# Kernel tuning notes

Measured on AMD Instinct MI355X. Metric: run time of the kernel, lower is better.

The kernel has to match this reference:

```python
import jax, jax.numpy as jnp
import numpy as np

K = 4  # number of processing steps (init kwarg)


def setup_inputs() -> dict:
    key = jax.random.key(0)
    ks = jax.random.split(key, 6)
    B, S, D = 4096, 8192, 512
    H = D  # hidden_size == input_size (residual h + f_x)
    scale = 1.0 / np.sqrt(H)
    return {
        "f_x": jax.random.normal(ks[0], (B, D), dtype=jnp.float32),
        "g_S": jax.random.normal(ks[1], (S, D), dtype=jnp.float32),
        # LSTM step: input f_x (size D), 'hidden' is concat([h, r]) of size 2H
        "W_ih": jax.random.uniform(ks[2], (4 * H, D), jnp.float32, -scale, scale),
        "W_hh": jax.random.uniform(ks[3], (4 * H, 2 * H), jnp.float32, -scale, scale),
        "b_ih": jax.random.uniform(ks[4], (4 * H,), jnp.float32, -scale, scale),
        "b_hh": jax.random.uniform(ks[5], (4 * H,), jnp.float32, -scale, scale),
    }


def _lstm_step(x, hidden, c, W_ih, W_hh, b_ih, b_hh):
    # gates: [B, 4H]; PyTorch LSTMCell gate order (i, f, g, o)
    gates = x @ W_ih.T + b_ih + hidden @ W_hh.T + b_hh
    i, f, g, o = jnp.split(gates, 4, axis=1)
    c_new = jax.nn.sigmoid(f) * c + jax.nn.sigmoid(i) * jnp.tanh(g)
    h_new = jax.nn.sigmoid(o) * jnp.tanh(c_new)
    return h_new, c_new


def reference(f_x, g_S, W_ih, W_hh, b_ih, b_hh):
    # f_x: [B, D] queries; g_S: [S, D] support set embeddings
    h = f_x
    c = jnp.zeros_like(f_x)
    for _ in range(K):
        a = jax.nn.softmax(h @ g_S.T, axis=1)       # [B, S] attention over support
        r = a @ g_S                                  # [B, D] attention readout
        concat = jnp.concatenate([h, r], axis=1)     # [B, 2D]
        h, c = _lstm_step(f_x, concat, c, W_ih, W_hh, b_ih, b_hh)
        h = h + f_x                                  # residual skip connection
    return h
```

## Files before the change

### kernel.cpp

```cpp
#include <hip/hip_runtime.h>

typedef _Float16 f16x8 __attribute__((ext_vector_type(8)));
typedef _Float16 f16x4 __attribute__((ext_vector_type(4)));
typedef float f32x4 __attribute__((ext_vector_type(4)));

#define S_DIM 8192
#define D_DIM 512

__device__ __forceinline__ void gload_lds16(const _Float16* g, _Float16* l) {
  __builtin_amdgcn_global_load_lds(
      (const __attribute__((address_space(1))) unsigned int*)g,
      (__attribute__((address_space(3))) unsigned int*)l, 16, 0, 0);
}

__device__ __forceinline__ float sigf(float x) { return 1.0f / (1.0f + __expf(-x)); }
__device__ __forceinline__ float tanhfast(float x) {
  return 1.0f - 2.0f / (__expf(2.0f * x) + 1.0f);
}


template <int BM, int BN>
__global__ __launch_bounds__(256) void gemm_bt(const _Float16* __restrict__ A, int lda,
                                               const _Float16* __restrict__ B, int ldb,
                                               _Float16* __restrict__ C, int ldc, int K) {
  constexpr int BK = 64;
  constexpr int FM = BM / 32, FN = BN / 32;
  __shared__ _Float16 As[BM * BK];
  __shared__ _Float16 Bs[BN * BK];
  const int tid = threadIdx.x;
  const int lane = tid & 63;
  const int wv = tid >> 6;
  const int bm = blockIdx.y * BM;
  const int bn = blockIdx.x * BN;
  const int wm = (wv >> 1) * (BM / 2);
  const int wn = (wv & 1) * (BN / 2);
  const int fr = lane & 15;
  const int hi4 = lane >> 4;
  const int rx7 = fr & 7;
  const int srow = lane >> 3;
  const int schk = (lane & 7) ^ srow;

  f32x4 acc[FM][FN] = {};

  for (int kt = 0; kt < K; kt += BK) {
    __syncthreads();
#pragma unroll
    for (int p = 0; p < BM / 32; ++p) {
      const int m = wv + 4 * p;
      gload_lds16(A + (size_t)(bm + 8 * m + srow) * lda + kt + schk * 8, As + 512 * m);
    }
#pragma unroll
    for (int p = 0; p < BN / 32; ++p) {
      const int m = wv + 4 * p;
      gload_lds16(B + (size_t)(bn + 8 * m + srow) * ldb + kt + schk * 8, Bs + 512 * m);
    }
    __syncthreads();

#pragma unroll
    for (int h = 0; h < 2; ++h) {
      const int co = (((h << 2) | hi4) ^ rx7) << 3;
      f16x8 af[FM], bf[FN];
#pragma unroll
      for (int i = 0; i < FM; ++i)
        af[i] = *(const f16x8*)&As[(wm + i * 16 + fr) * 64 + co];
#pragma unroll
      for (int j = 0; j < FN; ++j)
        bf[j] = *(const f16x8*)&Bs[(wn + j * 16 + fr) * 64 + co];
#pragma unroll
      for (int i = 0; i < FM; ++i)
#pragma unroll
        for (int j = 0; j < FN; ++j)
          acc[i][j] = __builtin_amdgcn_mfma_f32_16x16x32_f16(af[i], bf[j], acc[i][j], 0, 0, 0);
    }
  }

  const int cc = lane & 15;
  const int cr = (lane >> 4) * 4;
#pragma unroll
  for (int i = 0; i < FM; ++i)
#pragma unroll
    for (int j = 0; j < FN; ++j) {
      size_t base = (size_t)(bm + wm + i * 16 + cr) * ldc + (bn + wn + j * 16 + cc);
#pragma unroll
      for (int r = 0; r < 4; ++r) C[base + (size_t)r * ldc] = (_Float16)acc[i][j][r];
    }
}

__global__ __launch_bounds__(256) void gemm_rsplit(const _Float16* __restrict__ A,
                                                   const _Float16* __restrict__ B,
                                                   float* __restrict__ Ppart) {
  constexpr int BK = 64;
  __shared__ _Float16 As[128 * BK];
  __shared__ _Float16 Bs[64 * BK];
  const int tid = threadIdx.x;
  const int lane = tid & 63;
  const int wv = tid >> 6;
  const int bm = blockIdx.x * 128;
  const int bn = blockIdx.y * 64;
  const int kc = blockIdx.z;
  const int k0 = kc * 1024;
  const int wm = (wv >> 1) * 64;
  const int wn = (wv & 1) * 32;
  const int fr = lane & 15;
  const int hi4 = lane >> 4;
  const int rx7 = fr & 7;
  const int srow = lane >> 3;
  const int schk = (lane & 7) ^ srow;

  f32x4 acc[4][2] = {};

  for (int kt = k0; kt < k0 + 1024; kt += BK) {
    __syncthreads();
#pragma unroll
    for (int p = 0; p < 4; ++p) {
      const int m = wv + 4 * p;
      gload_lds16(A + (size_t)(bm + 8 * m + srow) * 16384 + kt + schk * 8, As + 512 * m);
    }
#pragma unroll
    for (int p = 0; p < 2; ++p) {
      const int m = wv + 4 * p;
      gload_lds16(B + (size_t)(bn + 8 * m + srow) * 8192 + kt + schk * 8, Bs + 512 * m);
    }
    __syncthreads();

#pragma unroll
    for (int h = 0; h < 2; ++h) {
      const int co = (((h << 2) | hi4) ^ rx7) << 3;
      f16x8 af[4], bf[2];
#pragma unroll
      for (int i = 0; i < 4; ++i)
        af[i] = *(const f16x8*)&As[(wm + i * 16 + fr) * 64 + co];
#pragma unroll
      for (int j = 0; j < 2; ++j)
        bf[j] = *(const f16x8*)&Bs[(wn + j * 16 + fr) * 64 + co];
#pragma unroll
      for (int i = 0; i < 4; ++i)
#pragma unroll
        for (int j = 0; j < 2; ++j)
          acc[i][j] = __builtin_amdgcn_mfma_f32_16x16x32_f16(af[i], bf[j], acc[i][j], 0, 0, 0);
    }
  }

  const int cc = lane & 15;
  const int cr = (lane >> 4) * 4;
#pragma unroll
  for (int i = 0; i < 4; ++i)
#pragma unroll
    for (int j = 0; j < 2; ++j) {
      size_t base = (size_t)(bm + wm + i * 16 + cr) * 8192 + 4096 + (size_t)kc * 512 +
                    (bn + wn + j * 16 + cc);
#pragma unroll
      for (int r = 0; r < 4; ++r) Ppart[base + (size_t)r * 8192] = acc[i][j][r];
    }
}

__global__ __launch_bounds__(256) void reduce_r(const float* __restrict__ Ppart,
                                                _Float16* __restrict__ rout) {
  int idx = blockIdx.x * 256 + threadIdx.x;
  int m = idx >> 7;
  int n4 = (idx & 127) * 4;
  const float* base = Ppart + (size_t)m * 8192 + 4096 + n4;
  f32x4 s = {0.f, 0.f, 0.f, 0.f};
#pragma unroll
  for (int kc = 0; kc < 8; ++kc) s += *(const f32x4*)(base + kc * 512);
  f16x4 h = {(_Float16)s[0], (_Float16)s[1], (_Float16)s[2], (_Float16)s[3]};
  *(f16x4*)&rout[(size_t)m * 1024 + n4] = h;
}

__global__ __launch_bounds__(256) void gemm_scores(const _Float16* __restrict__ Ah, int ldah,
                                                   const _Float16* __restrict__ Al,
                                                   const _Float16* __restrict__ Bh,
                                                   float* __restrict__ C) {
  constexpr int BK = 64;
  __shared__ _Float16 AsH[128 * BK];
  __shared__ _Float16 AsL[128 * BK];
  __shared__ _Float16 BsH[128 * BK];
  const int tid = threadIdx.x;
  const int lane = tid & 63;
  const int wv = tid >> 6;
  const int bm = blockIdx.y * 128;
  const int bn = blockIdx.x * 128;
  const int wm = (wv >> 1) * 64;
  const int wn = (wv & 1) * 64;
  const int fr = lane & 15;
  const int hi4 = lane >> 4;
  const int rx7 = fr & 7;
  const int srow = lane >> 3;
  const int schk = (lane & 7) ^ srow;

  f32x4 acc[4][4] = {};

  for (int kt = 0; kt < 512; kt += BK) {
    __syncthreads();
#pragma unroll
    for (int p = 0; p < 4; ++p) {
      const int m = wv + 4 * p;
      const int row = 8 * m + srow;
      gload_lds16(Ah + (size_t)(bm + row) * ldah + kt + schk * 8, AsH + 512 * m);
      gload_lds16(Al + (size_t)(bm + row) * 512 + kt + schk * 8, AsL + 512 * m);
      gload_lds16(Bh + (size_t)(bn + row) * 512 + kt + schk * 8, BsH + 512 * m);
    }
    __syncthreads();

#pragma unroll
    for (int h = 0; h < 2; ++h) {
      const int co = (((h << 2) | hi4) ^ rx7) << 3;
      f16x8 fah[4], fal[4], fbh[4];
#pragma unroll
      for (int i = 0; i < 4; ++i) {
        fah[i] = *(const f16x8*)&AsH[(wm + i * 16 + fr) * 64 + co];
        fal[i] = *(const f16x8*)&AsL[(wm + i * 16 + fr) * 64 + co];
        fbh[i] = *(const f16x8*)&BsH[(wn + i * 16 + fr) * 64 + co];
      }
#pragma unroll
      for (int i = 0; i < 4; ++i)
#pragma unroll
        for (int j = 0; j < 4; ++j) {
          acc[i][j] = __builtin_amdgcn_mfma_f32_16x16x32_f16(fah[i], fbh[j], acc[i][j], 0, 0, 0);
          acc[i][j] = __builtin_amdgcn_mfma_f32_16x16x32_f16(fal[i], fbh[j], acc[i][j], 0, 0, 0);
        }
    }
  }

  const int cc = lane & 15;
  const int cr = (lane >> 4) * 4;
#pragma unroll
  for (int i = 0; i < 4; ++i)
#pragma unroll
    for (int j = 0; j < 4; ++j) {
      size_t base = (size_t)(bm + wm + i * 16 + cr) * 8192 + (bn + wn + j * 16 + cc);
#pragma unroll
      for (int r = 0; r < 4; ++r) C[base + (size_t)r * 8192] = acc[i][j][r];
    }
}

__global__ __launch_bounds__(256) void prep_g(const float* __restrict__ g,
                                              _Float16* __restrict__ gT,
                                              _Float16* __restrict__ g_h) {
  __shared__ _Float16 tile[64][72];
  const int s0 = blockIdx.x * 64;
  const int d0 = blockIdx.y * 64;
  const int t = threadIdx.x;
  const int r = t >> 2;
  const int cq = (t & 3) * 16;
  alignas(16) _Float16 buf[16];
#pragma unroll
  for (int q = 0; q < 4; ++q) {
    f32x4 v = *(const f32x4*)&g[(size_t)(s0 + r) * D_DIM + d0 + cq + q * 4];
#pragma unroll
    for (int e = 0; e < 4; ++e) buf[q * 4 + e] = (_Float16)v[e];
  }
#pragma unroll
  for (int k = 0; k < 16; ++k) tile[r][cq + k] = buf[k];
  *(f16x8*)&g_h[(size_t)(s0 + r) * D_DIM + d0 + cq] = *(const f16x8*)&buf[0];
  *(f16x8*)&g_h[(size_t)(s0 + r) * D_DIM + d0 + cq + 8] = *(const f16x8*)&buf[8];
  __syncthreads();
  alignas(16) _Float16 ob[16];
#pragma unroll
  for (int k = 0; k < 16; ++k) ob[k] = tile[cq + k][r];
  *(f16x8*)&gT[(size_t)(d0 + r) * S_DIM + s0 + cq] = *(const f16x8*)&ob[0];
  *(f16x8*)&gT[(size_t)(d0 + r) * S_DIM + s0 + cq + 8] = *(const f16x8*)&ob[8];
}

__global__ __launch_bounds__(256) void prep_misc(const float* __restrict__ W_ih,
                                                 const float* __restrict__ W_hh,
                                                 const float* __restrict__ f_x,
                                                 _Float16* __restrict__ wih_h,
                                                 _Float16* __restrict__ whh_h,
                                                 _Float16* __restrict__ concat,
                                                 _Float16* __restrict__ h_lo,
                                                 float* __restrict__ c) {
  const int NW1 = 2048 * 512 / 4;
  const int NW2 = 2048 * 1024 / 4;
  const int NFX = 4096 * 512 / 4;
  int idx = blockIdx.x * 256 + threadIdx.x;
  if (idx < NW1) {
    f32x4 v = ((const f32x4*)W_ih)[idx];
    f16x4 h = {(_Float16)v[0], (_Float16)v[1], (_Float16)v[2], (_Float16)v[3]};
    ((f16x4*)wih_h)[idx] = h;
  } else if (idx < NW1 + NW2) {
    int k = idx - NW1;
    f32x4 v = ((const f32x4*)W_hh)[k];
    f16x4 h = {(_Float16)v[0], (_Float16)v[1], (_Float16)v[2], (_Float16)v[3]};
    ((f16x4*)whh_h)[k] = h;
  } else if (idx < NW1 + NW2 + NFX) {
    int k = idx - NW1 - NW2;
    f32x4 v = ((const f32x4*)f_x)[k];
    f16x4 h, lo;
#pragma unroll
    for (int e = 0; e < 4; ++e) {
      h[e] = (_Float16)v[e];
      lo[e] = (_Float16)(v[e] - (float)h[e]);
    }
    int m = k >> 7, j4 = k & 127;
    ((f16x4*)concat)[m * 256 + j4] = h;
    ((f16x4*)h_lo)[k] = lo;
    f32x4 z = {0.f, 0.f, 0.f, 0.f};
    ((f32x4*)c)[k] = z;
  }
}

__global__ __launch_bounds__(256) void softmax_inplace(float* __restrict__ P) {
  float* p = P + (size_t)blockIdx.x * S_DIM;
  const int tid = threadIdx.x, lane = tid & 63, wave = tid >> 6;
  __shared__ float red[8];
  float x[32];
#pragma unroll
  for (int i = 0; i < 8; ++i) {
    f32x4 v = *(const f32x4*)&p[i * 1024 + tid * 4];
#pragma unroll
    for (int j = 0; j < 4; ++j) x[i * 4 + j] = v[j];
  }
  float m = -3.0e38f;
#pragma unroll
  for (int k = 0; k < 32; ++k) m = fmaxf(m, x[k]);
#pragma unroll
  for (int o = 32; o; o >>= 1) m = fmaxf(m, __shfl_xor(m, o));
  if (lane == 0) red[wave] = m;
  __syncthreads();
  m = fmaxf(fmaxf(red[0], red[1]), fmaxf(red[2], red[3]));
  float s = 0.f;
#pragma unroll
  for (int k = 0; k < 32; ++k) {
    x[k] = exp2f((x[k] - m) * 1.44269504f);
    s += x[k];
  }
#pragma unroll
  for (int o = 32; o; o >>= 1) s += __shfl_xor(s, o);
  if (lane == 0) red[4 + wave] = s;
  __syncthreads();
  s = (red[4] + red[5]) + (red[6] + red[7]);
  float inv = 1.0f / s;
  _Float16* out = (_Float16*)p;
#pragma unroll
  for (int i = 0; i < 8; ++i) {
    f16x4 v;
#pragma unroll
    for (int j = 0; j < 4; ++j) v[j] = (_Float16)(x[i * 4 + j] * inv);
    *(f16x4*)&out[i * 1024 + tid * 4] = v;
  }
}

__global__ __launch_bounds__(256) void lstm_step(const _Float16* __restrict__ gmm,
                                                 const _Float16* __restrict__ gbase,
                                                 const float* __restrict__ b_ih,
                                                 const float* __restrict__ b_hh,
                                                 const float* __restrict__ f_x,
                                                 float* __restrict__ c,
                                                 _Float16* __restrict__ concat,
                                                 _Float16* __restrict__ h_lo,
                                                 float* __restrict__ hout) {
  int idx = blockIdx.x * 256 + threadIdx.x;
  int m = idx >> 7;
  int j = (idx & 127) * 4;
  size_t grow = (size_t)m * 2048 + j;
  f16x4 gI = *(const f16x4*)&gmm[grow];
  f16x4 gF = *(const f16x4*)&gmm[grow + 512];
  f16x4 gG = *(const f16x4*)&gmm[grow + 1024];
  f16x4 gO = *(const f16x4*)&gmm[grow + 1536];
  f16x4 aI = *(const f16x4*)&gbase[grow];
  f16x4 aF = *(const f16x4*)&gbase[grow + 512];
  f16x4 aG = *(const f16x4*)&gbase[grow + 1024];
  f16x4 aO = *(const f16x4*)&gbase[grow + 1536];
  f32x4 biI = *(const f32x4*)&b_ih[j];
  f32x4 biF = *(const f32x4*)&b_ih[j + 512];
  f32x4 biG = *(const f32x4*)&b_ih[j + 1024];
  f32x4 biO = *(const f32x4*)&b_ih[j + 1536];
  f32x4 bhI = *(const f32x4*)&b_hh[j];
  f32x4 bhF = *(const f32x4*)&b_hh[j + 512];
  f32x4 bhG = *(const f32x4*)&b_hh[j + 1024];
  f32x4 bhO = *(const f32x4*)&b_hh[j + 1536];
  f32x4 cv = ((const f32x4*)c)[idx];
  f32x4 fx = ((const f32x4*)f_x)[idx];
  f32x4 cn, hn;
  f16x4 h16, l16;
#pragma unroll
  for (int k = 0; k < 4; ++k) {
    float gi = (float)gI[k] + (float)aI[k] + biI[k] + bhI[k];
    float gf = (float)gF[k] + (float)aF[k] + biF[k] + bhF[k];
    float gg = (float)gG[k] + (float)aG[k] + biG[k] + bhG[k];
    float go = (float)gO[k] + (float)aO[k] + biO[k] + bhO[k];
    float ci = sigf(gf) * cv[k] + sigf(gi) * tanhfast(gg);
    float hi = sigf(go) * tanhfast(ci) + fx[k];
    cn[k] = ci;
    hn[k] = hi;
    h16[k] = (_Float16)hi;
    l16[k] = (_Float16)(hi - (float)h16[k]);
  }
  ((f32x4*)c)[idx] = cn;
  ((f32x4*)hout)[idx] = hn;
  ((f16x4*)concat)[m * 256 + (idx & 127)] = h16;
  ((f16x4*)h_lo)[idx] = l16;
}

extern "C" void kernel_launch(void* const* d_in, const int* in_sizes, int n_in,
                              void* d_out, int out_size, void* d_ws, size_t ws_size,
                              hipStream_t stream) {
  const float* f_x = (const float*)d_in[0];
  const float* g_S = (const float*)d_in[1];
  const float* W_ih = (const float*)d_in[2];
  const float* W_hh = (const float*)d_in[3];
  const float* b_ih = (const float*)d_in[4];
  const float* b_hh = (const float*)d_in[5];
  float* hout = (float*)d_out;

  char* w = (char*)d_ws;
  float* P32 = (float*)w;
  _Float16* gates = (_Float16*)w;
  _Float16* gbase = (_Float16*)(w + 67108864);
  _Float16* concat = (_Float16*)(w + 83886080);
  _Float16* g_h = (_Float16*)(w + 92274688);
  _Float16* gT = (_Float16*)(w + 109051904);
  _Float16* wih_h = (_Float16*)(w + 117440512);
  _Float16* whh_h = (_Float16*)(w + 119537664);
  float* c = (float*)(w + 123731968);
  _Float16* h_lo = (_Float16*)(w + 132120576);

  prep_g<<<dim3(S_DIM / 64, D_DIM / 64), 256, 0, stream>>>(g_S, gT, g_h);
  prep_misc<<<5120, 256, 0, stream>>>(W_ih, W_hh, f_x, wih_h, whh_h, concat, h_lo, c);

  gemm_bt<128, 128><<<dim3(2048 / 128, 4096 / 128), 256, 0, stream>>>(
      concat, 1024, wih_h, 512, gbase, 2048, 512);

  for (int it = 0; it < 4; ++it) {
    for (int hb = 0; hb < 2; ++hb) {
      const _Float16* hhi = concat + (size_t)hb * 2048 * 1024;
      const _Float16* hlo = h_lo + (size_t)hb * 2048 * 512;
      gemm_scores<<<dim3(64, 16), 256, 0, stream>>>(hhi, 1024, hlo, g_h, P32);
      softmax_inplace<<<2048, 256, 0, stream>>>(P32);
      gemm_rsplit<<<dim3(16, 8, 8), 256, 0, stream>>>((const _Float16*)P32, gT, P32);
      reduce_r<<<1024, 256, 0, stream>>>(P32, concat + (size_t)hb * 2048 * 1024 + 512);
    }
    gemm_bt<128, 128><<<dim3(2048 / 128, 4096 / 128), 256, 0, stream>>>(
        concat, 1024, whh_h, 1024, gates, 2048, 1024);
    lstm_step<<<2048, 256, 0, stream>>>(gates, gbase, b_ih, b_hh, f_x, c, concat, h_lo, hout);
  }
  (void)in_sizes; (void)n_in; (void)out_size; (void)ws_size;
}
```

Baseline: 870.8 us.

## Rewrite scores GEMM with 256x256 tiles, double-buffered LDS, and split-K hi/lo stages

Replaces the scores GEMM with a 512-thread kernel using 256x256 block tiles and double-buffered LDS, so global loads for the next K-tile overlap the MFMA work on the current one. Instead of loading hi and lo A fragments together in each step, K is treated as 16 tiles: the first 8 read the hi part and the last 8 read the lo part, both against the same B. MFMA sections are wrapped in s_setprio. This reuses each B tile over more rows and hides load latency. In exchange it uses more LDS and registers and launches only 256 blocks per call, which may lower occupancy.

```diff
diff --git a/kernel.cpp b/kernel.cpp
--- a/kernel.cpp
+++ b/kernel.cpp
@@ -167,65 +167,84 @@
   *(f16x4*)&rout[(size_t)m * 1024 + n4] = h;
 }
 
-__global__ __launch_bounds__(256) void gemm_scores(const _Float16* __restrict__ Ah, int ldah,
-                                                   const _Float16* __restrict__ Al,
-                                                   const _Float16* __restrict__ Bh,
-                                                   float* __restrict__ C) {
-  constexpr int BK = 64;
-  __shared__ _Float16 AsH[128 * BK];
-  __shared__ _Float16 AsL[128 * BK];
-  __shared__ _Float16 BsH[128 * BK];
+__global__ __launch_bounds__(512) void gemm_scores2(const _Float16* __restrict__ Ah,
+                                                    const _Float16* __restrict__ Al,
+                                                    const _Float16* __restrict__ Bh,
+                                                    float* __restrict__ C) {
+  __shared__ _Float16 As[2][256 * 64];
+  __shared__ _Float16 Bs[2][256 * 64];
   const int tid = threadIdx.x;
   const int lane = tid & 63;
   const int wv = tid >> 6;
-  const int bm = blockIdx.y * 128;
-  const int bn = blockIdx.x * 128;
-  const int wm = (wv >> 1) * 64;
-  const int wn = (wv & 1) * 64;
+  const int bm = blockIdx.y * 256;
+  const int bn = blockIdx.x * 256;
+  const int wm = (wv >> 2) * 128;
+  const int wn = (wv & 3) * 64;
   const int fr = lane & 15;
   const int hi4 = lane >> 4;
   const int rx7 = fr & 7;
   const int srow = lane >> 3;
   const int schk = (lane & 7) ^ srow;
 
-  f32x4 acc[4][4] = {};
-
-  for (int kt = 0; kt < 512; kt += BK) {
+  f32x4 acc[8][4] = {};
+
+  auto stage_q = [&](int t, int q, _Float16* nA, _Float16* nB) {
+    const int m = wv + 8 * q;
+    const int k0 = t * 64;
+    const _Float16* asrc =
+        (t < 8) ? Ah + (size_t)(bm + 8 * m + srow) * 1024 + k0 + schk * 8
+                : Al + (size_t)(bm + 8 * m + srow) * 512 + (k0 - 512) + schk * 8;
+    gload_lds16(asrc, nA + 512 * m);
+    gload_lds16(Bh + (size_t)(bn + 8 * m + srow) * 512 + (t & 7) * 64 + schk * 8,
+                nB + 512 * m);
+  };
+
+  auto tile = [&](int t, const _Float16* cA, const _Float16* cB, _Float16* nA,
+                  _Float16* nB) {
+#pragma unroll
+    for (int q = 0; q < 4; ++q) {
+      if (t < 15) stage_q(t + 1, q, nA, nB);
+      f16x8 af[2][2], bf[4][2];
+#pragma unroll
+      for (int ii = 0; ii < 2; ++ii)
+#pragma unroll
+        for (int h = 0; h < 2; ++h)
+          af[ii][h] = *(const f16x8*)&cA[(wm + (2 * q + ii) * 16 + fr) * 64 +
+                                         ((((h << 2) | hi4) ^ rx7) << 3)];
+#pragma unroll
+      for (int j = 0; j < 4; ++j)
+#pragma unroll
+        for (int h = 0; h < 2; ++h)
+          bf[j][h] = *(const f16x8*)&cB[(wn + j * 16 + fr) * 64 +
+                                        ((((h << 2) | hi4) ^ rx7) << 3)];
+      __builtin_amdgcn_s_setprio(1);
+#pragma unroll
+      for (int ii = 0; ii < 2; ++ii)
+#pragma unroll
+        for (int j = 0; j < 4; ++j) {
+          acc[2 * q + ii][j] = __builtin_amdgcn_mfma_f32_16x16x32_f16(
+              af[ii][0], bf[j][0], acc[2 * q + ii][j], 0, 0, 0);
+          acc[2 * q + ii][j] = __builtin_amdgcn_mfma_f32_16x16x32_f16(
+              af[ii][1], bf[j][1], acc[2 * q + ii][j], 0, 0, 0);
+        }
+      __builtin_amdgcn_s_setprio(0);
+    }
     __syncthreads();
-#pragma unroll
-    for (int p = 0; p < 4; ++p) {
-      const int m = wv + 4 * p;
-      const int row = 8 * m + srow;
-      gload_lds16(Ah + (size_t)(bm + row) * ldah + kt + schk * 8, AsH + 512 * m);
-      gload_lds16(Al + (size_t)(bm + row) * 512 + kt + schk * 8, AsL + 512 * m);
-      gload_lds16(Bh + (size_t)(bn + row) * 512 + kt + schk * 8, BsH + 512 * m);
-    }
-    __syncthreads();
-
-#pragma unroll
-    for (int h = 0; h < 2; ++h) {
-      const int co = (((h << 2) | hi4) ^ rx7) << 3;
-      f16x8 fah[4], fal[4], fbh[4];
-#pragma unroll
-      for (int i = 0; i < 4; ++i) {
-        fah[i] = *(const f16x8*)&AsH[(wm + i * 16 + fr) * 64 + co];
-        fal[i] = *(const f16x8*)&AsL[(wm + i * 16 + fr) * 64 + co];
-        fbh[i] = *(const f16x8*)&BsH[(wn + i * 16 + fr) * 64 + co];
-      }
-#pragma unroll
-      for (int i = 0; i < 4; ++i)
-#pragma unroll
-        for (int j = 0; j < 4; ++j) {
-          acc[i][j] = __builtin_amdgcn_mfma_f32_16x16x32_f16(fah[i], fbh[j], acc[i][j], 0, 0, 0);
-          acc[i][j] = __builtin_amdgcn_mfma_f32_16x16x32_f16(fal[i], fbh[j], acc[i][j], 0, 0, 0);
-        }
-    }
+  };
+
+#pragma unroll
+  for (int q = 0; q < 4; ++q) stage_q(0, q, As[0], Bs[0]);
+  __syncthreads();
+
+  for (int tt = 0; tt < 16; tt += 2) {
+    tile(tt, As[0], Bs[0], As[1], Bs[1]);
+    tile(tt + 1, As[1], Bs[1], As[0], Bs[0]);
   }
 
   const int cc = lane & 15;
   const int cr = (lane >> 4) * 4;
 #pragma unroll
-  for (int i = 0; i < 4; ++i)
+  for (int i = 0; i < 8; ++i)
 #pragma unroll
     for (int j = 0; j < 4; ++j) {
       size_t base = (size_t)(bm + wm + i * 16 + cr) * 8192 + (bn + wn + j * 16 + cc);
@@ -426,7 +445,7 @@
     for (int hb = 0; hb < 2; ++hb) {
       const _Float16* hhi = concat + (size_t)hb * 2048 * 1024;
       const _Float16* hlo = h_lo + (size_t)hb * 2048 * 512;
-      gemm_scores<<<dim3(64, 16), 256, 0, stream>>>(hhi, 1024, hlo, g_h, P32);
+      gemm_scores2<<<dim3(32, 8), 512, 0, stream>>>(hhi, hlo, g_h, P32);
       softmax_inplace<<<2048, 256, 0, stream>>>(P32);
       gemm_rsplit<<<dim3(16, 8, 8), 256, 0, stream>>>((const _Float16*)P32, gT, P32);
       reduce_r<<<1024, 256, 0, stream>>>(P32, concat + (size_t)hb * 2048 * 1024 + 512);
```

After: 887.0 us. Within noise of the previous version (+1.9%).

## Fuse hidden-to-gates GEMM with LSTM cell update and split h/r buffers

Applied to the files above, without the earlier changes.

Replaces the separate gates GEMM and elementwise lstm_step kernel with one gemm_gates kernel. Each block computes all four gate slices for 32 hidden columns, then applies the LSTM update directly in the epilogue, so the fp16 gates tensor is never written to or read back from memory. The concat buffer is split into ping-pong h buffers plus a separate r buffer, and the two biases are pre-summed once. The fused GEMM uses 128x128 tiles with no double-buffering and scalar epilogue stores, which may cost some GEMM efficiency.

```diff
diff --git a/kernel.cpp b/kernel.cpp
--- a/kernel.cpp
+++ b/kernel.cpp
@@ -164,7 +164,7 @@
 #pragma unroll
   for (int kc = 0; kc < 8; ++kc) s += *(const f32x4*)(base + kc * 512);
   f16x4 h = {(_Float16)s[0], (_Float16)s[1], (_Float16)s[2], (_Float16)s[3]};
-  *(f16x4*)&rout[(size_t)m * 1024 + n4] = h;
+  *(f16x4*)&rout[(size_t)m * 512 + n4] = h;
 }
 
 __global__ __launch_bounds__(256) void gemm_scores(const _Float16* __restrict__ Ah, int ldah,
@@ -234,6 +234,97 @@
     }
 }
 
+__global__ __launch_bounds__(256) void gemm_gates(const _Float16* __restrict__ Ah,
+                                                  const _Float16* __restrict__ Ar,
+                                                  const _Float16* __restrict__ B,
+                                                  const _Float16* __restrict__ gbase,
+                                                  const float* __restrict__ bsum,
+                                                  const float* __restrict__ f_x,
+                                                  float* __restrict__ c,
+                                                  _Float16* __restrict__ hnext,
+                                                  _Float16* __restrict__ h_lo,
+                                                  float* __restrict__ hout) {
+  __shared__ _Float16 As[128 * 64];
+  __shared__ _Float16 Bs[128 * 64];
+  const int tid = threadIdx.x;
+  const int lane = tid & 63;
+  const int wv = tid >> 6;
+  const int n0 = blockIdx.x * 32;
+  const int bm = blockIdx.y * 128;
+  const int fr = lane & 15;
+  const int hi4 = lane >> 4;
+  const int rx7 = fr & 7;
+  const int srow = lane >> 3;
+  const int schk = (lane & 7) ^ srow;
+
+  f32x4 acc[2][8] = {};
+
+  for (int t = 0; t < 16; ++t) {
+    const int kt = t * 64;
+    __syncthreads();
+#pragma unroll
+    for (int p = 0; p < 4; ++p) {
+      const int m = wv + 4 * p;
+      const int arow = bm + 8 * m + srow;
+      const _Float16* asrc = (t < 8)
+                                 ? Ah + (size_t)arow * 512 + kt + schk * 8
+                                 : Ar + (size_t)arow * 512 + (kt - 512) + schk * 8;
+      gload_lds16(asrc, As + 512 * m);
+      const int brow = 8 * m + srow;
+      const int wrow = ((brow >> 5) << 9) + n0 + (brow & 31);
+      gload_lds16(B + (size_t)wrow * 1024 + kt + schk * 8, Bs + 512 * m);
+    }
+    __syncthreads();
+
+#pragma unroll
+    for (int h = 0; h < 2; ++h) {
+      const int co = (((h << 2) | hi4) ^ rx7) << 3;
+      f16x8 af[2], bf[8];
+#pragma unroll
+      for (int i = 0; i < 2; ++i)
+        af[i] = *(const f16x8*)&As[(wv * 32 + i * 16 + fr) * 64 + co];
+#pragma unroll
+      for (int j = 0; j < 8; ++j)
+        bf[j] = *(const f16x8*)&Bs[(j * 16 + fr) * 64 + co];
+#pragma unroll
+      for (int i = 0; i < 2; ++i)
+#pragma unroll
+        for (int j = 0; j < 8; ++j)
+          acc[i][j] = __builtin_amdgcn_mfma_f32_16x16x32_f16(af[i], bf[j], acc[i][j], 0, 0, 0);
+    }
+  }
+
+  const int cc = lane & 15;
+  const int cr = (lane >> 4) * 4;
+#pragma unroll
+  for (int jj = 0; jj < 2; ++jj) {
+    const int colq = n0 + jj * 16 + cc;
+    const float bI = bsum[colq];
+    const float bF = bsum[colq + 512];
+    const float bG = bsum[colq + 1024];
+    const float bO = bsum[colq + 1536];
+#pragma unroll
+    for (int i = 0; i < 2; ++i)
+#pragma unroll
+      for (int r = 0; r < 4; ++r) {
+        const int row = bm + wv * 32 + i * 16 + cr + r;
+        const size_t g0 = (size_t)row * 2048 + colq;
+        const float gi = acc[i][jj][r] + (float)gbase[g0] + bI;
+        const float gf = acc[i][2 + jj][r] + (float)gbase[g0 + 512] + bF;
+        const float gg = acc[i][4 + jj][r] + (float)gbase[g0 + 1024] + bG;
+        const float go = acc[i][6 + jj][r] + (float)gbase[g0 + 1536] + bO;
+        const size_t o = (size_t)row * 512 + colq;
+        const float ci = sigf(gf) * c[o] + sigf(gi) * tanhfast(gg);
+        const float hi = sigf(go) * tanhfast(ci) + f_x[o];
+        c[o] = ci;
+        hout[o] = hi;
+        const _Float16 h16 = (_Float16)hi;
+        hnext[o] = h16;
+        h_lo[o] = (_Float16)(hi - (float)h16);
+      }
+  }
+}
+
 __global__ __launch_bounds__(256) void prep_g(const float* __restrict__ g,
                                               _Float16* __restrict__ gT,
                                               _Float16* __restrict__ g_h) {
@@ -265,11 +356,14 @@
 __global__ __launch_bounds__(256) void prep_misc(const float* __restrict__ W_ih,
                                                  const float* __restrict__ W_hh,
                                                  const float* __restrict__ f_x,
+                                                 const float* __restrict__ b_ih,
+                                                 const float* __restrict__ b_hh,
                                                  _Float16* __restrict__ wih_h,
                                                  _Float16* __restrict__ whh_h,
-                                                 _Float16* __restrict__ concat,
+                                                 _Float16* __restrict__ hbufA,
                                                  _Float16* __restrict__ h_lo,
-                                                 float* __restrict__ c) {
+                                                 float* __restrict__ c,
+                                                 float* __restrict__ bsum) {
   const int NW1 = 2048 * 512 / 4;
   const int NW2 = 2048 * 1024 / 4;
   const int NFX = 4096 * 512 / 4;
@@ -292,11 +386,15 @@
       h[e] = (_Float16)v[e];
       lo[e] = (_Float16)(v[e] - (float)h[e]);
     }
-    int m = k >> 7, j4 = k & 127;
-    ((f16x4*)concat)[m * 256 + j4] = h;
+    ((f16x4*)hbufA)[k] = h;
     ((f16x4*)h_lo)[k] = lo;
     f32x4 z = {0.f, 0.f, 0.f, 0.f};
     ((f32x4*)c)[k] = z;
+  } else if (idx < NW1 + NW2 + NFX + 512) {
+    int k = idx - NW1 - NW2 - NFX;
+    f32x4 bi = ((const f32x4*)b_ih)[k];
+    f32x4 bh = ((const f32x4*)b_hh)[k];
+    ((f32x4*)bsum)[k] = bi + bh;
   }
 }
 
@@ -339,58 +437,6 @@
     for (int j = 0; j < 4; ++j) v[j] = (_Float16)(x[i * 4 + j] * inv);
     *(f16x4*)&out[i * 1024 + tid * 4] = v;
   }
-}
-
-__global__ __launch_bounds__(256) void lstm_step(const _Float16* __restrict__ gmm,
-                                                 const _Float16* __restrict__ gbase,
-                                                 const float* __restrict__ b_ih,
-                                                 const float* __restrict__ b_hh,
-                                                 const float* __restrict__ f_x,
-                                                 float* __restrict__ c,
-                                                 _Float16* __restrict__ concat,
-                                                 _Float16* __restrict__ h_lo,
-                                                 float* __restrict__ hout) {
-  int idx = blockIdx.x * 256 + threadIdx.x;
-  int m = idx >> 7;
-  int j = (idx & 127) * 4;
-  size_t grow = (size_t)m * 2048 + j;
-  f16x4 gI = *(const f16x4*)&gmm[grow];
-  f16x4 gF = *(const f16x4*)&gmm[grow + 512];
-  f16x4 gG = *(const f16x4*)&gmm[grow + 1024];
-  f16x4 gO = *(const f16x4*)&gmm[grow + 1536];
-  f16x4 aI = *(const f16x4*)&gbase[grow];
-  f16x4 aF = *(const f16x4*)&gbase[grow + 512];
-  f16x4 aG = *(const f16x4*)&gbase[grow + 1024];
-  f16x4 aO = *(const f16x4*)&gbase[grow + 1536];
-  f32x4 biI = *(const f32x4*)&b_ih[j];
-  f32x4 biF = *(const f32x4*)&b_ih[j + 512];
-  f32x4 biG = *(const f32x4*)&b_ih[j + 1024];
-  f32x4 biO = *(const f32x4*)&b_ih[j + 1536];
-  f32x4 bhI = *(const f32x4*)&b_hh[j];
-  f32x4 bhF = *(const f32x4*)&b_hh[j + 512];
-  f32x4 bhG = *(const f32x4*)&b_hh[j + 1024];
-  f32x4 bhO = *(const f32x4*)&b_hh[j + 1536];
-  f32x4 cv = ((const f32x4*)c)[idx];
-  f32x4 fx = ((const f32x4*)f_x)[idx];
-  f32x4 cn, hn;
-  f16x4 h16, l16;
-#pragma unroll
-  for (int k = 0; k < 4; ++k) {
-    float gi = (float)gI[k] + (float)aI[k] + biI[k] + bhI[k];
-    float gf = (float)gF[k] + (float)aF[k] + biF[k] + bhF[k];
-    float gg = (float)gG[k] + (float)aG[k] + biG[k] + bhG[k];
-    float go = (float)gO[k] + (float)aO[k] + biO[k] + bhO[k];
-    float ci = sigf(gf) * cv[k] + sigf(gi) * tanhfast(gg);
-    float hi = sigf(go) * tanhfast(ci) + fx[k];
-    cn[k] = ci;
-    hn[k] = hi;
-    h16[k] = (_Float16)hi;
-    l16[k] = (_Float16)(hi - (float)h16[k]);
-  }
-  ((f32x4*)c)[idx] = cn;
-  ((f32x4*)hout)[idx] = hn;
-  ((f16x4*)concat)[m * 256 + (idx & 127)] = h16;
-  ((f16x4*)h_lo)[idx] = l16;
 }
 
 extern "C" void kernel_launch(void* const* d_in, const int* in_sizes, int n_in,
@@ -406,10 +452,12 @@
 
   char* w = (char*)d_ws;
   float* P32 = (float*)w;
-  _Float16* gates = (_Float16*)w;
   _Float16* gbase = (_Float16*)(w + 67108864);
-  _Float16* concat = (_Float16*)(w + 83886080);
+  _Float16* hbufA = (_Float16*)(w + 83886080);
+  _Float16* hbufB = (_Float16*)(w + 88080384);
   _Float16* g_h = (_Float16*)(w + 92274688);
+  _Float16* rbuf = (_Float16*)(w + 100663296);
+  float* bsum = (float*)(w + 104857600);
   _Float16* gT = (_Float16*)(w + 109051904);
   _Float16* wih_h = (_Float16*)(w + 117440512);
   _Float16* whh_h = (_Float16*)(w + 119537664);
@@ -417,23 +465,25 @@
   _Float16* h_lo = (_Float16*)(w + 132120576);
 
   prep_g<<<dim3(S_DIM / 64, D_DIM / 64), 256, 0, stream>>>(g_S, gT, g_h);
-  prep_misc<<<5120, 256, 0, stream>>>(W_ih, W_hh, f_x, wih_h, whh_h, concat, h_lo, c);
+  prep_misc<<<5122, 256, 0, stream>>>(W_ih, W_hh, f_x, b_ih, b_hh, wih_h, whh_h,
+                                      hbufA, h_lo, c, bsum);
 
   gemm_bt<128, 128><<<dim3(2048 / 128, 4096 / 128), 256, 0, stream>>>(
-      concat, 1024, wih_h, 512, gbase, 2048, 512);
+      hbufA, 512, wih_h, 512, gbase, 2048, 512);
 
   for (int it = 0; it < 4; ++it) {
+    _Float16* hcur = (it & 1) ? hbufB : hbufA;
+    _Float16* hnxt = (it & 1) ? hbufA : hbufB;
     for (int hb = 0; hb < 2; ++hb) {
-      const _Float16* hhi = concat + (size_t)hb * 2048 * 1024;
+      const _Float16* hhi = hcur + (size_t)hb * 2048 * 512;
       const _Float16* hlo = h_lo + (size_t)hb * 2048 * 512;
-      gemm_scores<<<dim3(64, 16), 256, 0, stream>>>(hhi, 1024, hlo, g_h, P32);
+      gemm_scores<<<dim3(64, 16), 256, 0, stream>>>(hhi, 512, hlo, g_h, P32);
       softmax_inplace<<<2048, 256, 0, stream>>>(P32);
       gemm_rsplit<<<dim3(16, 8, 8), 256, 0, stream>>>((const _Float16*)P32, gT, P32);
-      reduce_r<<<1024, 256, 0, stream>>>(P32, concat + (size_t)hb * 2048 * 1024 + 512);
-    }
-    gemm_bt<128, 128><<<dim3(2048 / 128, 4096 / 128), 256, 0, stream>>>(
-        concat, 1024, whh_h, 1024, gates, 2048, 1024);
-    lstm_step<<<2048, 256, 0, stream>>>(gates, gbase, b_ih, b_hh, f_x, c, concat, h_lo, hout);
+      reduce_r<<<1024, 256, 0, stream>>>(P32, rbuf + (size_t)hb * 2048 * 512);
+    }
+    gemm_gates<<<dim3(16, 32), 256, 0, stream>>>(hcur, rbuf, whh_h, gbase, bsum,
+                                                 f_x, c, hnxt, h_lo, hout);
   }
   (void)in_sizes; (void)n_in; (void)out_size; (void)ws_size;
 }
```

New measurement: 855.7 us. No clear change (-1.7%).
